# Kernel optimization log

Measured on AMD Instinct MI355X. Metric: run time of the kernel, lower is better.

Reference implementation:

```python
import jax, jax.numpy as jnp
import numpy as np

B, H, W, C, G = 256, 64, 64, 3, 128
MH, INV = 10, 18
AS = MH + INV  # 28
EPS = 1e-5


def _bn(x, g, b):
    # training-mode BatchNorm2d: batch stats over (N,H,W), biased variance
    m = x.mean((0, 2, 3), keepdims=True)
    v = x.var((0, 2, 3), keepdims=True)
    return (x - m) * jax.lax.rsqrt(v + EPS) * g.reshape(1, -1, 1, 1) + b.reshape(1, -1, 1, 1)


def _ln(x, g, b):
    m = x.mean(-1, keepdims=True)
    v = x.var(-1, keepdims=True)
    return (x - m) * jax.lax.rsqrt(v + EPS) * g + b


def _conv(x, w, pad):
    return jax.lax.conv_general_dilated(x, w, (1, 1), [(pad, pad), (pad, pad)],
                                        dimension_numbers=('NCHW', 'OIHW', 'NCHW'))


def setup_inputs() -> dict:
    key = jax.random.key(0)
    ks = jax.random.split(key, 24)
    r = lambda i, shape, s=1.0: jax.random.normal(ks[i], shape, jnp.float32) * s
    return {
        'agent_state': r(0, (B, AS)),
        'world_state': r(1, (B, C, H, W)),
        'action': jax.random.uniform(ks[2], (B, 15), jnp.float32, 0.0, 2.999),
        # cnn params
        'bn1_g': jnp.ones((C,), jnp.float32), 'bn1_b': jnp.zeros((C,), jnp.float32),
        'conv1_w': r(3, (G, C, 1, 1), 0.5),
        'bn2_g': jnp.ones((G,), jnp.float32), 'bn2_b': jnp.zeros((G,), jnp.float32),
        'conv2_w': r(4, (G, G, 3, 3), 0.05),
        'bn3_g': jnp.ones((G,), jnp.float32), 'bn3_b': jnp.zeros((G,), jnp.float32),
        'fc1_w': r(5, (20, G), 0.1), 'fc1_b': r(6, (20,), 0.1),
        # mh_inventory
        'ln_mi_g': jnp.ones((AS,), jnp.float32), 'ln_mi_b': jnp.zeros((AS,), jnp.float32),
        'mi_w1': r(7, (100, AS), 0.2), 'mi_w2': r(8, (20, 100), 0.2),
        # action embeddings
        'emb_craft': r(9, (5, 3)), 'emb_equip': r(10, (8, 3)),
        'emb_ncraft': r(11, (8, 3)), 'emb_nsmelt': r(12, (3, 2)), 'emb_place': r(13, (7, 3)),
        # combined_actions
        'ln_ca_g': jnp.ones((24,), jnp.float32), 'ln_ca_b': jnp.zeros((24,), jnp.float32),
        'ca_w1': r(14, (100, 24), 0.2), 'ca_b1': r(15, (100,), 0.1),
        'ca_w2': r(16, (20, 100), 0.2), 'ca_b2': r(17, (20,), 0.1),
        # combined
        'ln_c_g': jnp.ones((60,), jnp.float32), 'ln_c_b': jnp.zeros((60,), jnp.float32),
        'c_w': r(18, (1, 60), 0.2),
        # dist_net
        'ln_d_g': jnp.ones((2 * AS,), jnp.float32), 'ln_d_b': jnp.zeros((2 * AS,), jnp.float32),
        'd_w1': r(19, (50, 2 * AS), 0.2), 'd_w2': r(20, (1, 50), 0.2),
    }


def reference(agent_state, world_state, action,
              bn1_g, bn1_b, conv1_w, bn2_g, bn2_b, conv2_w, bn3_g, bn3_b,
              fc1_w, fc1_b, ln_mi_g, ln_mi_b, mi_w1, mi_w2,
              emb_craft, emb_equip, emb_ncraft, emb_nsmelt, emb_place,
              ln_ca_g, ln_ca_b, ca_w1, ca_b1, ca_w2, ca_b2,
              ln_c_g, ln_c_b, c_w, ln_d_g, ln_d_b, d_w1, d_w2):
    relu = jax.nn.relu
    # ---- CNN branch ----
    x = relu(_bn(world_state, bn1_g, bn1_b))
    x = _conv(x, conv1_w, 0)                      # [B,G,H,W]
    x = relu(_bn(x, bn2_g, bn2_b))
    x = _conv(x, conv2_w, 1)                      # [B,G,H,W]
    x = x.mean((2, 3), keepdims=True)             # AvgPool2d((H,W)) -> [B,G,1,1]
    x = relu(_bn(x, bn3_g, bn3_b)).reshape(x.shape[0], -1)  # [B,G]
    x = relu(x @ fc1_w.T + fc1_b)                 # [B,20]
    # ---- agent-state MLP ----
    y = relu(relu(_ln(agent_state, ln_mi_g, ln_mi_b) @ mi_w1.T) @ mi_w2.T)  # [B,20]
    # ---- per-action embeddings / identities (ModuleDict order) ----
    ai = jax.lax.stop_gradient(action).astype(jnp.int32)
    parts = [action[:, 0:1], action[:, 1:2], action[:, 2:3], action[:, 3:4],
             emb_craft[ai[:, 4]], emb_equip[ai[:, 5]],
             action[:, 6:7], action[:, 7:8], action[:, 8:9],
             emb_ncraft[ai[:, 9]], emb_nsmelt[ai[:, 10]], emb_place[ai[:, 11]],
             action[:, 12:13], action[:, 13:14], action[:, 14:15]]
    acts = jnp.concatenate(parts, axis=1)         # [B,24]
    z = relu(relu(_ln(acts, ln_ca_g, ln_ca_b) @ ca_w1.T + ca_b1) @ ca_w2.T + ca_b2)  # [B,20]
    # ---- combined head ----
    c = jnp.tanh(_ln(jnp.concatenate([x, y, z], axis=1), ln_c_g, ln_c_b) @ c_w.T)    # [B,1]
    # ---- dist_net (previous_agent_state starts as zeros) ----
    prev = jnp.zeros_like(agent_state)
    sc = jnp.concatenate([prev, agent_state], axis=1)  # [B,2*AS]
    d = jnp.tanh(jnp.tanh(_ln(sc, ln_d_g, ln_d_b) @ d_w1.T) @ d_w2.T)                # [B,1]
    return (c, d)
```

## Files before the change

### kernel.cpp

```cpp
#include <hip/hip_runtime.h>
#include <math.h>

#define EPSF 1e-5f

constexpr int OFF_RED1 = 0;
constexpr int OFF_A1B1 = 384;
constexpr int OFF_RED2 = 512;
constexpr int OFF_W2E  = 4096;
constexpr int OFF_M    = OFF_W2E + 128 * 128 * 9;

__device__ __forceinline__ float wave_sum(float v) {
    #pragma unroll
    for (int off = 32; off > 0; off >>= 1) v += __shfl_down(v, off);
    return v;
}

__global__ __launch_bounds__(256) void kA(const float* __restrict__ x,
                                          const float* __restrict__ w2,
                                          float* __restrict__ red1,
                                          float* __restrict__ w2e) {
    int blk = blockIdx.x, tid = threadIdx.x;
    if (blk < 192) {
        int c = blk % 3, seg = blk / 3;
        float s = 0.f, s2 = 0.f;
        for (int bb = 0; bb < 4; ++bb) {
            int b = seg * 4 + bb;
            const float4* p = (const float4*)(x + (size_t)(b * 3 + c) * 4096);
            for (int i = tid; i < 1024; i += 256) {
                float4 v = p[i];
                s += v.x + v.y + v.z + v.w;
                s2 = fmaf(v.x, v.x, s2); s2 = fmaf(v.y, v.y, s2);
                s2 = fmaf(v.z, v.z, s2); s2 = fmaf(v.w, v.w, s2);
            }
        }
        __shared__ float ls[4], ls2[4];
        float ws_ = wave_sum(s), ws2_ = wave_sum(s2);
        if ((tid & 63) == 0) { ls[tid >> 6] = ws_; ls2[tid >> 6] = ws2_; }
        __syncthreads();
        if (tid == 0) {
            red1[blk * 2 + 0] = ls[0] + ls[1] + ls[2] + ls[3];
            red1[blk * 2 + 1] = ls2[0] + ls2[1] + ls2[2] + ls2[3];
        }
    } else {
        int idx = (blk - 192) * 256 + tid;
        int g = idx >> 7, gp = idx & 127;
        const float* wp = w2 + (size_t)(g * 128 + gp) * 9;
        float v0 = wp[0], v1 = wp[1], v2 = wp[2], v3 = wp[3], v4 = wp[4],
              v5 = wp[5], v6 = wp[6], v7 = wp[7], v8 = wp[8];
        float c[9];
        c[0] = ((v0 + v1) + (v2 + v3)) + ((v4 + v5) + (v6 + v7)) + v8;
        c[1] = -(v6 + v7 + v8);
        c[2] = -(v0 + v1 + v2);
        c[3] = -(v2 + v5 + v8);
        c[4] = -(v0 + v3 + v6);
        c[5] = v8; c[6] = v6; c[7] = v2; c[8] = v0;
        #pragma unroll
        for (int k = 0; k < 9; ++k) {
            int jj = gp * 9 + k;
            w2e[(size_t)(jj >> 2) * 512 + g * 4 + (jj & 3)] = c[k];
        }
    }
}

__global__ __launch_bounds__(256) void kB(const float* __restrict__ x,
                                          const float* __restrict__ red1,
                                          const float* __restrict__ g1,
                                          const float* __restrict__ b1,
                                          float* __restrict__ red2,
                                          float* __restrict__ a1b1) {
    __shared__ float ab[6];
    int b = blockIdx.x, tid = threadIdx.x;
    if (tid < 3) {
        float s = 0.f, s2 = 0.f;
        for (int seg = 0; seg < 64; ++seg) {
            s  += red1[(seg * 3 + tid) * 2 + 0];
            s2 += red1[(seg * 3 + tid) * 2 + 1];
        }
        float n = 256.f * 4096.f;
        float mean = s / n, var = s2 / n - mean * mean;
        float a = g1[tid] * rsqrtf(var + EPSF);
        ab[tid] = a; ab[3 + tid] = b1[tid] - mean * a;
        if (b == 0) { a1b1[tid] = a; a1b1[3 + tid] = ab[3 + tid]; }
    }
    __syncthreads();
    float A0 = ab[0], A1 = ab[1], A2 = ab[2];
    float B0 = ab[3], B1 = ab[4], B2 = ab[5];
    float acc[9] = {0, 0, 0, 0, 0, 0, 0, 0, 0};
    const float4* p0 = (const float4*)(x + (size_t)(b * 3 + 0) * 4096);
    const float4* p1 = (const float4*)(x + (size_t)(b * 3 + 1) * 4096);
    const float4* p2 = (const float4*)(x + (size_t)(b * 3 + 2) * 4096);
    for (int i = tid; i < 1024; i += 256) {
        float4 v0 = p0[i], v1 = p1[i], v2 = p2[i];
        #define MOM(e) { \
            float t0 = fmaxf(0.f, fmaf(A0, v0.e, B0)); \
            float t1 = fmaxf(0.f, fmaf(A1, v1.e, B1)); \
            float t2 = fmaxf(0.f, fmaf(A2, v2.e, B2)); \
            acc[0] += t0; acc[1] += t1; acc[2] += t2; \
            acc[3] = fmaf(t0, t0, acc[3]); acc[4] = fmaf(t0, t1, acc[4]); \
            acc[5] = fmaf(t0, t2, acc[5]); acc[6] = fmaf(t1, t1, acc[6]); \
            acc[7] = fmaf(t1, t2, acc[7]); acc[8] = fmaf(t2, t2, acc[8]); }
        MOM(x) MOM(y) MOM(z) MOM(w)
        #undef MOM
    }
    __shared__ float lw[4][9];
    #pragma unroll
    for (int k = 0; k < 9; ++k) {
        float v = wave_sum(acc[k]);
        if ((tid & 63) == 0) lw[tid >> 6][k] = v;
    }
    __syncthreads();
    if (tid == 0) {
        #pragma unroll
        for (int k = 0; k < 9; ++k)
            red2[b * 9 + k] = lw[0][k] + lw[1][k] + lw[2][k] + lw[3][k];
    }
}

__global__ __launch_bounds__(512) void kC(const float* __restrict__ x,
                                          const float* __restrict__ red2,
                                          const float* __restrict__ w1,
                                          const float* __restrict__ g2,
                                          const float* __restrict__ b2,
                                          const float* __restrict__ a1b1,
                                          const float* __restrict__ w2e,
                                          float* __restrict__ m) {
    __shared__ __align__(16) float lds[12288];
    __shared__ __align__(16) float Fsh[1152];
    __shared__ float wt[384], bt[128], momp[288], mom[9], ab[6];
    int b = blockIdx.x, tid = threadIdx.x;
    if (tid < 6) ab[tid] = a1b1[tid];
    if (tid < 288) {
        int seg = tid / 9, k = tid - seg * 9;
        float s = 0.f;
        #pragma unroll
        for (int r = 0; r < 8; ++r) s += red2[(seg * 8 + r) * 9 + k];
        momp[tid] = s;
    }
    __syncthreads();
    if (tid < 9) {
        float s = 0.f;
        #pragma unroll
        for (int sg = 0; sg < 32; ++sg) s += momp[sg * 9 + tid];
        mom[tid] = s / (256.f * 4096.f);
    }
    {
        float A0 = ab[0], A1 = ab[1], A2 = ab[2];
        float B0 = ab[3], B1 = ab[4], B2 = ab[5];
        const float4* xb = (const float4*)(x + (size_t)b * 3 * 4096);
        for (int i = tid; i < 3072; i += 512) {
            float4 v = xb[i];
            int c = i >> 10;
            float a = (c == 0) ? A0 : ((c == 1) ? A1 : A2);
            float bb = (c == 0) ? B0 : ((c == 1) ? B1 : B2);
            v.x = fmaxf(0.f, fmaf(a, v.x, bb));
            v.y = fmaxf(0.f, fmaf(a, v.y, bb));
            v.z = fmaxf(0.f, fmaf(a, v.z, bb));
            v.w = fmaxf(0.f, fmaf(a, v.w, bb));
            *(float4*)&lds[i << 2] = v;
        }
    }
    __syncthreads();
    if (tid < 128) {
        int g = tid;
        float wa = w1[g * 3 + 0], wb = w1[g * 3 + 1], wc = w1[g * 3 + 2];
        float mean = wa * mom[0] + wb * mom[1] + wc * mom[2];
        float ey2 = wa * wa * mom[3] + wb * wb * mom[6] + wc * wc * mom[8]
                  + 2.f * (wa * wb * mom[4] + wa * wc * mom[5] + wb * wc * mom[7]);
        float var = ey2 - mean * mean;
        float a = g2[g] * rsqrtf(var + EPSF);
        wt[g * 3 + 0] = a * wa; wt[g * 3 + 1] = a * wb; wt[g * 3 + 2] = a * wc;
        bt[g] = b2[g] - mean * a;
    }
    __syncthreads();
    int gl = tid & 31, q = tid >> 5;
    {
        float w0[4], w1v[4], w2v[4], bw[4], S[4] = {0, 0, 0, 0};
        #pragma unroll
        for (int j = 0; j < 4; ++j) {
            int g = gl + 32 * j;
            w0[j] = wt[g * 3 + 0]; w1v[j] = wt[g * 3 + 1];
            w2v[j] = wt[g * 3 + 2]; bw[j] = bt[g];
        }
        int base = q * 256;
        #pragma unroll 4
        for (int i = 0; i < 64; ++i) {
            int pp = base + i * 4;
            float4 t0 = *(const float4*)&lds[pp];
            float4 t1 = *(const float4*)&lds[4096 + pp];
            float4 t2 = *(const float4*)&lds[8192 + pp];
            #pragma unroll
            for (int j = 0; j < 4; ++j) {
                float u0 = fmaxf(0.f, fmaf(w0[j], t0.x, fmaf(w1v[j], t1.x, fmaf(w2v[j], t2.x, bw[j]))));
                float u1 = fmaxf(0.f, fmaf(w0[j], t0.y, fmaf(w1v[j], t1.y, fmaf(w2v[j], t2.y, bw[j]))));
                float u2 = fmaxf(0.f, fmaf(w0[j], t0.z, fmaf(w1v[j], t1.z, fmaf(w2v[j], t2.z, bw[j]))));
                float u3 = fmaxf(0.f, fmaf(w0[j], t0.w, fmaf(w1v[j], t1.w, fmaf(w2v[j], t2.w, bw[j]))));
                S[j] += (u0 + u1) + (u2 + u3);
            }
        }
        {
            int g = tid & 127, task = tid >> 7;
            float vw0 = wt[g * 3 + 0], vw1 = wt[g * 3 + 1], vw2 = wt[g * 3 + 2], vb = bt[g];
            float s = 0.f, first = 0.f, last = 0.f;
            int p0 = (task == 1) ? 63 * 64 : ((task == 3) ? 63 : 0);
            int stp = (task >= 2) ? 64 : 1;
            #pragma unroll 4
            for (int i = 0; i < 64; ++i) {
                int p = p0 + i * stp;
                float u = fmaxf(0.f, fmaf(vw0, lds[p], fmaf(vw1, lds[4096 + p], fmaf(vw2, lds[8192 + p], vb))));
                s += u;
                if (i == 0) first = u;
                if (i == 63) last = u;
            }
            Fsh[g * 9 + 1 + task] = s;
            if (task == 0) { Fsh[g * 9 + 5] = first; Fsh[g * 9 + 6] = last; }
            if (task == 1) { Fsh[g * 9 + 7] = first; Fsh[g * 9 + 8] = last; }
        }
        __syncthreads();
        #pragma unroll
        for (int j = 0; j < 4; ++j) lds[(gl + 32 * j) * 17 + q] = S[j];
    }
    __syncthreads();
    if (tid < 128) {
        float s = 0.f;
        #pragma unroll
        for (int qq = 0; qq < 16; ++qq) s += lds[tid * 17 + qq];
        Fsh[tid * 9 + 0] = s;
    }
    __syncthreads();
    {
        int chunk = tid >> 7, g = tid & 127;
        float acc = 0.f;
        #pragma unroll 4
        for (int t = 0; t < 72; ++t) {
            int jb = chunk * 72 + t;
            float4 wv = *(const float4*)&w2e[(size_t)jb * 512 + g * 4];
            float4 fv = *(const float4*)&Fsh[jb * 4];
            acc = fmaf(wv.x, fv.x, fmaf(wv.y, fv.y, fmaf(wv.z, fv.z, fmaf(wv.w, fv.w, acc))));
        }
        __syncthreads();
        lds[chunk * 128 + g] = acc;
    }
    __syncthreads();
    if (tid < 128)
        m[b * 128 + tid] = (lds[tid] + lds[128 + tid] + lds[256 + tid] + lds[384 + tid]) * (1.f / 4096.f);
}

__global__ __launch_bounds__(256) void kE(
    const float* __restrict__ m, const float* __restrict__ g3, const float* __restrict__ b3,
    const float* __restrict__ agent, const float* __restrict__ action,
    const float* __restrict__ fc1w, const float* __restrict__ fc1b,
    const float* __restrict__ lnmig, const float* __restrict__ lnmib,
    const float* __restrict__ miw1, const float* __restrict__ miw2,
    const float* __restrict__ embc, const float* __restrict__ embe,
    const float* __restrict__ embnc, const float* __restrict__ embns,
    const float* __restrict__ embp,
    const float* __restrict__ lncag, const float* __restrict__ lncab,
    const float* __restrict__ caw1, const float* __restrict__ cab1,
    const float* __restrict__ caw2, const float* __restrict__ cab2,
    const float* __restrict__ lncg, const float* __restrict__ lncb,
    const float* __restrict__ cw,
    const float* __restrict__ lndg, const float* __restrict__ lndb,
    const float* __restrict__ dw1, const float* __restrict__ dw2,
    float* __restrict__ out) {
    __shared__ float red[4][128];
    __shared__ float xsh[128];
    __shared__ float lnv[28], lnca[24], lnsc[56], h1[100], h2[100], h3[50], cat[60];
    int b = blockIdx.x, tid = threadIdx.x;
    {
        int g = tid & 127, half = tid >> 7;
        float s = 0.f, s2 = 0.f;
        for (int i = 0; i < 128; ++i) {
            float v = m[(half * 128 + i) * 128 + g];
            s += v; s2 = fmaf(v, v, s2);
        }
        red[half * 2 + 0][g] = s;
        red[half * 2 + 1][g] = s2;
    }
    __syncthreads();
    if (tid < 128) {
        float s = red[0][tid] + red[2][tid], s2 = red[1][tid] + red[3][tid];
        float mean = s / 256.f, var = s2 / 256.f - mean * mean;
        float a = g3[tid] * rsqrtf(var + EPSF);
        float bb = b3[tid] - mean * a;
        xsh[tid] = fmaxf(0.f, fmaf(a, m[b * 128 + tid], bb));
    }
    int l = tid & 63, w = tid >> 6;
    if (w == 0) {
        float av = (l < 28) ? agent[b * 28 + l] : 0.f;
        float s = wave_sum(av), s2 = wave_sum(av * av);
        s = __shfl(s, 0); s2 = __shfl(s2, 0);
        float mean = s / 28.f, var = s2 / 28.f - mean * mean;
        float rs = rsqrtf(var + EPSF);
        if (l < 28) lnv[l] = (av - mean) * rs * lnmig[l] + lnmib[l];
    } else if (w == 1) {
        const float* ab = action + b * 15;
        float actv = 0.f;
        if (l < 24) {
            if (l < 4)       actv = ab[l];
            else if (l < 7)  { int ix = (int)ab[4];  actv = embc[ix * 3 + (l - 4)]; }
            else if (l < 10) { int ix = (int)ab[5];  actv = embe[ix * 3 + (l - 7)]; }
            else if (l < 13) actv = ab[l - 4];
            else if (l < 16) { int ix = (int)ab[9];  actv = embnc[ix * 3 + (l - 13)]; }
            else if (l < 18) { int ix = (int)ab[10]; actv = embns[ix * 2 + (l - 16)]; }
            else if (l < 21) { int ix = (int)ab[11]; actv = embp[ix * 3 + (l - 18)]; }
            else             actv = ab[l - 9];
        }
        float s = wave_sum(actv), s2 = wave_sum(actv * actv);
        s = __shfl(s, 0); s2 = __shfl(s2, 0);
        float mean = s / 24.f, var = s2 / 24.f - mean * mean;
        float rs = rsqrtf(var + EPSF);
        if (l < 24) lnca[l] = (actv - mean) * rs * lncag[l] + lncab[l];
    } else if (w == 2) {
        float g1v = (l < 56) ? agent[b * 28 + (l < 28 ? l : l - 28)] : 0.f;
        float av = (l < 28) ? g1v : 0.f;
        float s = wave_sum(av), s2 = wave_sum(av * av);
        s = __shfl(s, 0); s2 = __shfl(s2, 0);
        float mean = s / 56.f, var = s2 / 56.f - mean * mean;
        float rs = rsqrtf(var + EPSF);
        if (l < 56) {
            float vv = (l < 28) ? 0.f : g1v;
            lnsc[l] = (vv - mean) * rs * lndg[l] + lndb[l];
        }
    }
    __syncthreads();
    if (tid < 100) {
        float a = 0.f;
        for (int i = 0; i < 28; ++i) a = fmaf(miw1[tid * 28 + i], lnv[i], a);
        h1[tid] = fmaxf(0.f, a);
    } else if (tid < 200) {
        int j = tid - 100;
        float a = cab1[j];
        for (int i = 0; i < 24; ++i) a = fmaf(caw1[j * 24 + i], lnca[i], a);
        h2[j] = fmaxf(0.f, a);
    } else if (tid < 250) {
        int j = tid - 200;
        float a = 0.f;
        for (int i = 0; i < 56; ++i) a = fmaf(dw1[j * 56 + i], lnsc[i], a);
        h3[j] = tanhf(a);
    }
    __syncthreads();
    if (tid < 20) {
        float a = 0.f;
        for (int i = 0; i < 100; ++i) a = fmaf(miw2[tid * 100 + i], h1[i], a);
        cat[20 + tid] = fmaxf(0.f, a);
    } else if (tid >= 64 && tid < 84) {
        int j = tid - 64;
        float a = cab2[j];
        for (int i = 0; i < 100; ++i) a = fmaf(caw2[j * 100 + i], h2[i], a);
        cat[40 + j] = fmaxf(0.f, a);
    } else if (tid >= 128 && tid < 148) {
        int j = tid - 128;
        float a = fc1b[j];
        for (int i = 0; i < 128; ++i) a = fmaf(fc1w[j * 128 + i], xsh[i], a);
        cat[j] = fmaxf(0.f, a);
    } else if (tid >= 192) {
        int l3 = tid - 192;
        float dt = (l3 < 50) ? dw2[l3] * h3[l3] : 0.f;
        dt = wave_sum(dt);
        if (l3 == 0) out[256 + b] = tanhf(dt);
    }
    __syncthreads();
    if (w == 0) {
        float cv = (l < 60) ? cat[l] : 0.f;
        float ss = wave_sum(cv), ss2 = wave_sum(cv * cv);
        ss = __shfl(ss, 0); ss2 = __shfl(ss2, 0);
        float mean60 = ss / 60.f, var60 = ss2 / 60.f - mean60 * mean60;
        float rs60 = rsqrtf(var60 + EPSF);
        float term = (l < 60) ? cw[l] * ((cv - mean60) * rs60 * lncg[l] + lncb[l]) : 0.f;
        term = wave_sum(term);
        if (l == 0) out[b] = tanhf(term);
    }
}

extern "C" void kernel_launch(void* const* d_in, const int* in_sizes, int n_in,
                              void* d_out, int out_size, void* d_ws, size_t ws_size,
                              hipStream_t stream) {
    (void)in_sizes; (void)n_in; (void)out_size; (void)ws_size;
    const float* agent  = (const float*)d_in[0];
    const float* world  = (const float*)d_in[1];
    const float* action = (const float*)d_in[2];
    const float* bn1_g  = (const float*)d_in[3];
    const float* bn1_b  = (const float*)d_in[4];
    const float* conv1w = (const float*)d_in[5];
    const float* bn2_g  = (const float*)d_in[6];
    const float* bn2_b  = (const float*)d_in[7];
    const float* conv2w = (const float*)d_in[8];
    const float* bn3_g  = (const float*)d_in[9];
    const float* bn3_b  = (const float*)d_in[10];
    const float* fc1w   = (const float*)d_in[11];
    const float* fc1b   = (const float*)d_in[12];
    const float* lnmig  = (const float*)d_in[13];
    const float* lnmib  = (const float*)d_in[14];
    const float* miw1   = (const float*)d_in[15];
    const float* miw2   = (const float*)d_in[16];
    const float* embc   = (const float*)d_in[17];
    const float* embe   = (const float*)d_in[18];
    const float* embnc  = (const float*)d_in[19];
    const float* embns  = (const float*)d_in[20];
    const float* embp   = (const float*)d_in[21];
    const float* lncag  = (const float*)d_in[22];
    const float* lncab  = (const float*)d_in[23];
    const float* caw1   = (const float*)d_in[24];
    const float* cab1   = (const float*)d_in[25];
    const float* caw2   = (const float*)d_in[26];
    const float* cab2   = (const float*)d_in[27];
    const float* lncg   = (const float*)d_in[28];
    const float* lncb   = (const float*)d_in[29];
    const float* cw     = (const float*)d_in[30];
    const float* lndg   = (const float*)d_in[31];
    const float* lndb   = (const float*)d_in[32];
    const float* dw1    = (const float*)d_in[33];
    const float* dw2    = (const float*)d_in[34];
    float* out = (float*)d_out;
    float* ws = (float*)d_ws;

    hipLaunchKernelGGL(kA, dim3(256), dim3(256), 0, stream,
                       world, conv2w, ws + OFF_RED1, ws + OFF_W2E);
    hipLaunchKernelGGL(kB, dim3(256), dim3(256), 0, stream,
                       world, ws + OFF_RED1, bn1_g, bn1_b, ws + OFF_RED2, ws + OFF_A1B1);
    hipLaunchKernelGGL(kC, dim3(256), dim3(512), 0, stream,
                       world, ws + OFF_RED2, conv1w, bn2_g, bn2_b, ws + OFF_A1B1,
                       ws + OFF_W2E, ws + OFF_M);
    hipLaunchKernelGGL(kE, dim3(256), dim3(256), 0, stream,
                       ws + OFF_M, bn3_g, bn3_b, agent, action, fc1w, fc1b,
                       lnmig, lnmib, miw1, miw2,
                       embc, embe, embnc, embns, embp,
                       lncag, lncab, caw1, cab1, caw2, cab2,
                       lncg, lncb, cw, lndg, lndb, dw1, dw2, out);
}
```

Before: 186.3 us.

## Fuse four kernels into one cooperative kernel with grid syncs

Replaces the four-kernel pipeline with a single cooperative kernel of 256 blocks by 512 threads that uses grid.sync between the BN-stat, moment, conv and head stages. Each block keeps its batch item's normalized input in shared memory, so the second pass over the world tensor in the conv stage is no longer needed. This removes launch gaps and some global traffic, but needs all 256 blocks co-resident and adds grid-wide barrier cost. If the cooperative launch fails, it falls back to the old kernels.

```diff
diff --git a/kernel.cpp b/kernel.cpp
--- a/kernel.cpp
+++ b/kernel.cpp
@@ -1,5 +1,8 @@
 #include <hip/hip_runtime.h>
+#include <hip/hip_cooperative_groups.h>
 #include <math.h>
+
+namespace cg = cooperative_groups;
 
 #define EPSF 1e-5f
 
@@ -13,6 +16,335 @@
     #pragma unroll
     for (int off = 32; off > 0; off >>= 1) v += __shfl_down(v, off);
     return v;
+}
+
+struct KParams {
+    const float *agent, *world, *action;
+    const float *bn1_g, *bn1_b, *conv1w, *bn2_g, *bn2_b, *conv2w, *bn3_g, *bn3_b;
+    const float *fc1w, *fc1b, *lnmig, *lnmib, *miw1, *miw2;
+    const float *embc, *embe, *embnc, *embns, *embp;
+    const float *lncag, *lncab, *caw1, *cab1, *caw2, *cab2;
+    const float *lncg, *lncb, *cw, *lndg, *lndb, *dw1, *dw2;
+    float *out, *ws;
+};
+
+__global__ __launch_bounds__(512, 2) void fused(KParams p) {
+    cg::grid_group grid = cg::this_grid();
+    const int blk = blockIdx.x, tid = threadIdx.x;
+    float* red1 = p.ws + OFF_RED1;
+    float* red2 = p.ws + OFF_RED2;
+    float* w2e  = p.ws + OFF_W2E;
+    float* m    = p.ws + OFF_M;
+
+    __shared__ __align__(16) float T[12288];
+    __shared__ __align__(16) float Fsh[1152];
+    __shared__ float wt[384], bt[128], momp[288], mom[9], ab[6];
+    __shared__ float wred[8][9], lss[8], lss2[8], mrow[128];
+    __shared__ float xsh[128], lnv[28], lnca[24], lnsc[56], h1[100], h2[100], h3[50], cat[60];
+
+    if (blk < 192) {
+        int c = blk % 3, seg = blk / 3;
+        float s = 0.f, s2 = 0.f;
+        #pragma unroll
+        for (int bb = 0; bb < 4; ++bb) {
+            const float4* q = (const float4*)(p.world + (size_t)((seg * 4 + bb) * 3 + c) * 4096);
+            for (int i = tid; i < 1024; i += 512) {
+                float4 v = q[i];
+                s += (v.x + v.y) + (v.z + v.w);
+                s2 = fmaf(v.x, v.x, s2); s2 = fmaf(v.y, v.y, s2);
+                s2 = fmaf(v.z, v.z, s2); s2 = fmaf(v.w, v.w, s2);
+            }
+        }
+        float a = wave_sum(s), b2_ = wave_sum(s2);
+        if ((tid & 63) == 0) { lss[tid >> 6] = a; lss2[tid >> 6] = b2_; }
+        __syncthreads();
+        if (tid == 0) {
+            float ts = 0.f, ts2 = 0.f;
+            #pragma unroll
+            for (int wv = 0; wv < 8; ++wv) { ts += lss[wv]; ts2 += lss2[wv]; }
+            red1[blk * 2 + 0] = ts; red1[blk * 2 + 1] = ts2;
+        }
+    } else if (tid < 256) {
+        int idx = (blk - 192) * 256 + tid;
+        int g = idx >> 7, gp = idx & 127;
+        const float* wp = p.conv2w + (size_t)(g * 128 + gp) * 9;
+        float v0 = wp[0], v1 = wp[1], v2 = wp[2], v3 = wp[3], v4 = wp[4],
+              v5 = wp[5], v6 = wp[6], v7 = wp[7], v8 = wp[8];
+        float c9[9];
+        c9[0] = ((v0 + v1) + (v2 + v3)) + ((v4 + v5) + (v6 + v7)) + v8;
+        c9[1] = -(v6 + v7 + v8);
+        c9[2] = -(v0 + v1 + v2);
+        c9[3] = -(v2 + v5 + v8);
+        c9[4] = -(v0 + v3 + v6);
+        c9[5] = v8; c9[6] = v6; c9[7] = v2; c9[8] = v0;
+        #pragma unroll
+        for (int k = 0; k < 9; ++k) {
+            int jj = gp * 9 + k;
+            w2e[(size_t)(jj >> 2) * 512 + g * 4 + (jj & 3)] = c9[k];
+        }
+    }
+    grid.sync();
+
+    const int b = blk;
+    if (tid < 3) {
+        float s = 0.f, s2 = 0.f;
+        for (int seg = 0; seg < 64; ++seg) {
+            s  += red1[(seg * 3 + tid) * 2 + 0];
+            s2 += red1[(seg * 3 + tid) * 2 + 1];
+        }
+        float n = 256.f * 4096.f;
+        float mean = s / n, var = s2 / n - mean * mean;
+        float a = p.bn1_g[tid] * rsqrtf(var + EPSF);
+        ab[tid] = a; ab[3 + tid] = p.bn1_b[tid] - mean * a;
+    }
+    __syncthreads();
+    {
+        float A0 = ab[0], A1 = ab[1], A2 = ab[2];
+        float B0 = ab[3], B1 = ab[4], B2 = ab[5];
+        const float4* p0 = (const float4*)(p.world + (size_t)(b * 3 + 0) * 4096);
+        const float4* p1 = (const float4*)(p.world + (size_t)(b * 3 + 1) * 4096);
+        const float4* p2 = (const float4*)(p.world + (size_t)(b * 3 + 2) * 4096);
+        float acc[9] = {0, 0, 0, 0, 0, 0, 0, 0, 0};
+        for (int i = tid; i < 1024; i += 512) {
+            float4 v0 = p0[i], v1 = p1[i], v2 = p2[i];
+            float4 t0, t1, t2;
+            #define MOM(e) { \
+                float u0 = fmaxf(0.f, fmaf(A0, v0.e, B0)); \
+                float u1 = fmaxf(0.f, fmaf(A1, v1.e, B1)); \
+                float u2 = fmaxf(0.f, fmaf(A2, v2.e, B2)); \
+                t0.e = u0; t1.e = u1; t2.e = u2; \
+                acc[0] += u0; acc[1] += u1; acc[2] += u2; \
+                acc[3] = fmaf(u0, u0, acc[3]); acc[4] = fmaf(u0, u1, acc[4]); \
+                acc[5] = fmaf(u0, u2, acc[5]); acc[6] = fmaf(u1, u1, acc[6]); \
+                acc[7] = fmaf(u1, u2, acc[7]); acc[8] = fmaf(u2, u2, acc[8]); }
+            MOM(x) MOM(y) MOM(z) MOM(w)
+            #undef MOM
+            *(float4*)&T[i * 4]        = t0;
+            *(float4*)&T[4096 + i * 4] = t1;
+            *(float4*)&T[8192 + i * 4] = t2;
+        }
+        #pragma unroll
+        for (int k = 0; k < 9; ++k) {
+            float v = wave_sum(acc[k]);
+            if ((tid & 63) == 0) wred[tid >> 6][k] = v;
+        }
+        __syncthreads();
+        if (tid < 9) {
+            float s = 0.f;
+            #pragma unroll
+            for (int wv = 0; wv < 8; ++wv) s += wred[wv][tid];
+            red2[b * 9 + tid] = s;
+        }
+    }
+    grid.sync();
+
+    if (tid < 288) {
+        int seg = tid / 9, k = tid - seg * 9;
+        float s = 0.f;
+        #pragma unroll
+        for (int r = 0; r < 8; ++r) s += red2[(seg * 8 + r) * 9 + k];
+        momp[tid] = s;
+    }
+    __syncthreads();
+    if (tid < 9) {
+        float s = 0.f;
+        #pragma unroll
+        for (int sg = 0; sg < 32; ++sg) s += momp[sg * 9 + tid];
+        mom[tid] = s / (256.f * 4096.f);
+    }
+    __syncthreads();
+    if (tid < 128) {
+        int g = tid;
+        float wa = p.conv1w[g * 3 + 0], wb = p.conv1w[g * 3 + 1], wc = p.conv1w[g * 3 + 2];
+        float mean = wa * mom[0] + wb * mom[1] + wc * mom[2];
+        float ey2 = wa * wa * mom[3] + wb * wb * mom[6] + wc * wc * mom[8]
+                  + 2.f * (wa * wb * mom[4] + wa * wc * mom[5] + wb * wc * mom[7]);
+        float var = ey2 - mean * mean;
+        float a = p.bn2_g[g] * rsqrtf(var + EPSF);
+        wt[g * 3 + 0] = a * wa; wt[g * 3 + 1] = a * wb; wt[g * 3 + 2] = a * wc;
+        bt[g] = p.bn2_b[g] - mean * a;
+    }
+    __syncthreads();
+    int gl = tid & 31, qc = tid >> 5;
+    {
+        float w0[4], w1v[4], w2v[4], bw[4], S[4] = {0, 0, 0, 0};
+        #pragma unroll
+        for (int j = 0; j < 4; ++j) {
+            int g = gl + 32 * j;
+            w0[j] = wt[g * 3 + 0]; w1v[j] = wt[g * 3 + 1];
+            w2v[j] = wt[g * 3 + 2]; bw[j] = bt[g];
+        }
+        int base = qc * 256;
+        #pragma unroll 4
+        for (int i = 0; i < 64; ++i) {
+            int pp = base + i * 4;
+            float4 t0 = *(const float4*)&T[pp];
+            float4 t1 = *(const float4*)&T[4096 + pp];
+            float4 t2 = *(const float4*)&T[8192 + pp];
+            #pragma unroll
+            for (int j = 0; j < 4; ++j) {
+                float u0 = fmaxf(0.f, fmaf(w0[j], t0.x, fmaf(w1v[j], t1.x, fmaf(w2v[j], t2.x, bw[j]))));
+                float u1 = fmaxf(0.f, fmaf(w0[j], t0.y, fmaf(w1v[j], t1.y, fmaf(w2v[j], t2.y, bw[j]))));
+                float u2 = fmaxf(0.f, fmaf(w0[j], t0.z, fmaf(w1v[j], t1.z, fmaf(w2v[j], t2.z, bw[j]))));
+                float u3 = fmaxf(0.f, fmaf(w0[j], t0.w, fmaf(w1v[j], t1.w, fmaf(w2v[j], t2.w, bw[j]))));
+                S[j] += (u0 + u1) + (u2 + u3);
+            }
+        }
+        {
+            int g = tid & 127, task = tid >> 7;
+            float vw0 = wt[g * 3 + 0], vw1 = wt[g * 3 + 1], vw2 = wt[g * 3 + 2], vb = bt[g];
+            float s = 0.f, first = 0.f, last = 0.f;
+            int p0 = (task == 1) ? 63 * 64 : ((task == 3) ? 63 : 0);
+            int stp = (task >= 2) ? 64 : 1;
+            #pragma unroll 4
+            for (int i = 0; i < 64; ++i) {
+                int pp = p0 + i * stp;
+                float u = fmaxf(0.f, fmaf(vw0, T[pp], fmaf(vw1, T[4096 + pp], fmaf(vw2, T[8192 + pp], vb))));
+                s += u;
+                if (i == 0) first = u;
+                if (i == 63) last = u;
+            }
+            Fsh[g * 9 + 1 + task] = s;
+            if (task == 0) { Fsh[g * 9 + 5] = first; Fsh[g * 9 + 6] = last; }
+            if (task == 1) { Fsh[g * 9 + 7] = first; Fsh[g * 9 + 8] = last; }
+        }
+        __syncthreads();
+        #pragma unroll
+        for (int j = 0; j < 4; ++j) T[(gl + 32 * j) * 17 + qc] = S[j];
+    }
+    __syncthreads();
+    if (tid < 128) {
+        float s = 0.f;
+        #pragma unroll
+        for (int qq = 0; qq < 16; ++qq) s += T[tid * 17 + qq];
+        Fsh[tid * 9 + 0] = s;
+    }
+    __syncthreads();
+    {
+        int chunk = tid >> 7, g = tid & 127;
+        float acc = 0.f;
+        #pragma unroll 4
+        for (int t = 0; t < 72; ++t) {
+            int jb = chunk * 72 + t;
+            float4 wv = *(const float4*)&w2e[(size_t)jb * 512 + g * 4];
+            float4 fv = *(const float4*)&Fsh[jb * 4];
+            acc = fmaf(wv.x, fv.x, fmaf(wv.y, fv.y, fmaf(wv.z, fv.z, fmaf(wv.w, fv.w, acc))));
+        }
+        __syncthreads();
+        T[chunk * 128 + g] = acc;
+    }
+    __syncthreads();
+    if (tid < 128) {
+        float v = (T[tid] + T[128 + tid] + T[256 + tid] + T[384 + tid]) * (1.f / 4096.f);
+        m[b * 128 + tid] = v;
+        mrow[tid] = v;
+    }
+    grid.sync();
+
+    {
+        int g = tid & 127, qtr = tid >> 7;
+        float s = 0.f, s2 = 0.f;
+        for (int i = 0; i < 64; ++i) {
+            float v = m[(qtr * 64 + i) * 128 + g];
+            s += v; s2 = fmaf(v, v, s2);
+        }
+        T[tid] = s; T[512 + tid] = s2;
+    }
+    __syncthreads();
+    if (tid < 128) {
+        float s  = T[tid] + T[128 + tid] + T[256 + tid] + T[384 + tid];
+        float s2 = T[512 + tid] + T[640 + tid] + T[768 + tid] + T[896 + tid];
+        float mean = s / 256.f, var = s2 / 256.f - mean * mean;
+        float a = p.bn3_g[tid] * rsqrtf(var + EPSF);
+        float bb = p.bn3_b[tid] - mean * a;
+        xsh[tid] = fmaxf(0.f, fmaf(a, mrow[tid], bb));
+    }
+    int l = tid & 63, w = tid >> 6;
+    if (w == 0) {
+        float av = (l < 28) ? p.agent[b * 28 + l] : 0.f;
+        float s = wave_sum(av), s2 = wave_sum(av * av);
+        s = __shfl(s, 0); s2 = __shfl(s2, 0);
+        float mean = s / 28.f, var = s2 / 28.f - mean * mean;
+        float rs = rsqrtf(var + EPSF);
+        if (l < 28) lnv[l] = (av - mean) * rs * p.lnmig[l] + p.lnmib[l];
+    } else if (w == 1) {
+        const float* ap = p.action + b * 15;
+        float actv = 0.f;
+        if (l < 24) {
+            if (l < 4)       actv = ap[l];
+            else if (l < 7)  { int ix = (int)ap[4];  actv = p.embc[ix * 3 + (l - 4)]; }
+            else if (l < 10) { int ix = (int)ap[5];  actv = p.embe[ix * 3 + (l - 7)]; }
+            else if (l < 13) actv = ap[l - 4];
+            else if (l < 16) { int ix = (int)ap[9];  actv = p.embnc[ix * 3 + (l - 13)]; }
+            else if (l < 18) { int ix = (int)ap[10]; actv = p.embns[ix * 2 + (l - 16)]; }
+            else if (l < 21) { int ix = (int)ap[11]; actv = p.embp[ix * 3 + (l - 18)]; }
+            else             actv = ap[l - 9];
+        }
+        float s = wave_sum(actv), s2 = wave_sum(actv * actv);
+        s = __shfl(s, 0); s2 = __shfl(s2, 0);
+        float mean = s / 24.f, var = s2 / 24.f - mean * mean;
+        float rs = rsqrtf(var + EPSF);
+        if (l < 24) lnca[l] = (actv - mean) * rs * p.lncag[l] + p.lncab[l];
+    } else if (w == 2) {
+        float g1v = (l < 56) ? p.agent[b * 28 + (l < 28 ? l : l - 28)] : 0.f;
+        float av = (l < 28) ? g1v : 0.f;
+        float s = wave_sum(av), s2 = wave_sum(av * av);
+        s = __shfl(s, 0); s2 = __shfl(s2, 0);
+        float mean = s / 56.f, var = s2 / 56.f - mean * mean;
+        float rs = rsqrtf(var + EPSF);
+        if (l < 56) {
+            float vv = (l < 28) ? 0.f : g1v;
+            lnsc[l] = (vv - mean) * rs * p.lndg[l] + p.lndb[l];
+        }
+    }
+    __syncthreads();
+    if (tid < 100) {
+        float a = 0.f;
+        for (int i = 0; i < 28; ++i) a = fmaf(p.miw1[tid * 28 + i], lnv[i], a);
+        h1[tid] = fmaxf(0.f, a);
+    } else if (tid < 200) {
+        int j = tid - 100;
+        float a = p.cab1[j];
+        for (int i = 0; i < 24; ++i) a = fmaf(p.caw1[j * 24 + i], lnca[i], a);
+        h2[j] = fmaxf(0.f, a);
+    } else if (tid < 250) {
+        int j = tid - 200;
+        float a = 0.f;
+        for (int i = 0; i < 56; ++i) a = fmaf(p.dw1[j * 56 + i], lnsc[i], a);
+        h3[j] = tanhf(a);
+    }
+    __syncthreads();
+    if (tid < 20) {
+        float a = 0.f;
+        for (int i = 0; i < 100; ++i) a = fmaf(p.miw2[tid * 100 + i], h1[i], a);
+        cat[20 + tid] = fmaxf(0.f, a);
+    } else if (tid >= 64 && tid < 84) {
+        int j = tid - 64;
+        float a = p.cab2[j];
+        for (int i = 0; i < 100; ++i) a = fmaf(p.caw2[j * 100 + i], h2[i], a);
+        cat[40 + j] = fmaxf(0.f, a);
+    } else if (tid >= 128 && tid < 148) {
+        int j = tid - 128;
+        float a = p.fc1b[j];
+        for (int i = 0; i < 128; ++i) a = fmaf(p.fc1w[j * 128 + i], xsh[i], a);
+        cat[j] = fmaxf(0.f, a);
+    } else if (tid >= 192 && tid < 256) {
+        int l3 = tid - 192;
+        float dt = (l3 < 50) ? p.dw2[l3] * h3[l3] : 0.f;
+        dt = wave_sum(dt);
+        if (l3 == 0) p.out[256 + b] = tanhf(dt);
+    }
+    __syncthreads();
+    if (w == 0) {
+        float cv = (l < 60) ? cat[l] : 0.f;
+        float ss = wave_sum(cv), ss2 = wave_sum(cv * cv);
+        ss = __shfl(ss, 0); ss2 = __shfl(ss2, 0);
+        float mean60 = ss / 60.f, var60 = ss2 / 60.f - mean60 * mean60;
+        float rs60 = rsqrtf(var60 + EPSF);
+        float term = (l < 60) ? p.cw[l] * ((cv - mean60) * rs60 * p.lncg[l] + p.lncb[l]) : 0.f;
+        term = wave_sum(term);
+        if (l == 0) p.out[b] = tanhf(term);
+    }
 }
 
 __global__ __launch_bounds__(256) void kA(const float* __restrict__ x,
@@ -376,55 +708,62 @@
                               void* d_out, int out_size, void* d_ws, size_t ws_size,
                               hipStream_t stream) {
     (void)in_sizes; (void)n_in; (void)out_size; (void)ws_size;
-    const float* agent  = (const float*)d_in[0];
-    const float* world  = (const float*)d_in[1];
-    const float* action = (const float*)d_in[2];
-    const float* bn1_g  = (const float*)d_in[3];
-    const float* bn1_b  = (const float*)d_in[4];
-    const float* conv1w = (const float*)d_in[5];
-    const float* bn2_g  = (const float*)d_in[6];
-    const float* bn2_b  = (const float*)d_in[7];
-    const float* conv2w = (const float*)d_in[8];
-    const float* bn3_g  = (const float*)d_in[9];
-    const float* bn3_b  = (const float*)d_in[10];
-    const float* fc1w   = (const float*)d_in[11];
-    const float* fc1b   = (const float*)d_in[12];
-    const float* lnmig  = (const float*)d_in[13];
-    const float* lnmib  = (const float*)d_in[14];
-    const float* miw1   = (const float*)d_in[15];
-    const float* miw2   = (const float*)d_in[16];
-    const float* embc   = (const float*)d_in[17];
-    const float* embe   = (const float*)d_in[18];
-    const float* embnc  = (const float*)d_in[19];
-    const float* embns  = (const float*)d_in[20];
-    const float* embp   = (const float*)d_in[21];
-    const float* lncag  = (const float*)d_in[22];
-    const float* lncab  = (const float*)d_in[23];
-    const float* caw1   = (const float*)d_in[24];
-    const float* cab1   = (const float*)d_in[25];
-    const float* caw2   = (const float*)d_in[26];
-    const float* cab2   = (const float*)d_in[27];
-    const float* lncg   = (const float*)d_in[28];
-    const float* lncb   = (const float*)d_in[29];
-    const float* cw     = (const float*)d_in[30];
-    const float* lndg   = (const float*)d_in[31];
-    const float* lndb   = (const float*)d_in[32];
-    const float* dw1    = (const float*)d_in[33];
-    const float* dw2    = (const float*)d_in[34];
-    float* out = (float*)d_out;
-    float* ws = (float*)d_ws;
-
-    hipLaunchKernelGGL(kA, dim3(256), dim3(256), 0, stream,
-                       world, conv2w, ws + OFF_RED1, ws + OFF_W2E);
-    hipLaunchKernelGGL(kB, dim3(256), dim3(256), 0, stream,
-                       world, ws + OFF_RED1, bn1_g, bn1_b, ws + OFF_RED2, ws + OFF_A1B1);
-    hipLaunchKernelGGL(kC, dim3(256), dim3(512), 0, stream,
-                       world, ws + OFF_RED2, conv1w, bn2_g, bn2_b, ws + OFF_A1B1,
-                       ws + OFF_W2E, ws + OFF_M);
-    hipLaunchKernelGGL(kE, dim3(256), dim3(256), 0, stream,
-                       ws + OFF_M, bn3_g, bn3_b, agent, action, fc1w, fc1b,
-                       lnmig, lnmib, miw1, miw2,
-                       embc, embe, embnc, embns, embp,
-                       lncag, lncab, caw1, cab1, caw2, cab2,
-                       lncg, lncb, cw, lndg, lndb, dw1, dw2, out);
+    KParams hp;
+    hp.agent  = (const float*)d_in[0];
+    hp.world  = (const float*)d_in[1];
+    hp.action = (const float*)d_in[2];
+    hp.bn1_g  = (const float*)d_in[3];
+    hp.bn1_b  = (const float*)d_in[4];
+    hp.conv1w = (const float*)d_in[5];
+    hp.bn2_g  = (const float*)d_in[6];
+    hp.bn2_b  = (const float*)d_in[7];
+    hp.conv2w = (const float*)d_in[8];
+    hp.bn3_g  = (const float*)d_in[9];
+    hp.bn3_b  = (const float*)d_in[10];
+    hp.fc1w   = (const float*)d_in[11];
+    hp.fc1b   = (const float*)d_in[12];
+    hp.lnmig  = (const float*)d_in[13];
+    hp.lnmib  = (const float*)d_in[14];
+    hp.miw1   = (const float*)d_in[15];
+    hp.miw2   = (const float*)d_in[16];
+    hp.embc   = (const float*)d_in[17];
+    hp.embe   = (const float*)d_in[18];
+    hp.embnc  = (const float*)d_in[19];
+    hp.embns  = (const float*)d_in[20];
+    hp.embp   = (const float*)d_in[21];
+    hp.lncag  = (const float*)d_in[22];
+    hp.lncab  = (const float*)d_in[23];
+    hp.caw1   = (const float*)d_in[24];
+    hp.cab1   = (const float*)d_in[25];
+    hp.caw2   = (const float*)d_in[26];
+    hp.cab2   = (const float*)d_in[27];
+    hp.lncg   = (const float*)d_in[28];
+    hp.lncb   = (const float*)d_in[29];
+    hp.cw     = (const float*)d_in[30];
+    hp.lndg   = (const float*)d_in[31];
+    hp.lndb   = (const float*)d_in[32];
+    hp.dw1    = (const float*)d_in[33];
+    hp.dw2    = (const float*)d_in[34];
+    hp.out = (float*)d_out;
+    hp.ws  = (float*)d_ws;
+
+    void* args[] = {&hp};
+    hipError_t err = hipLaunchCooperativeKernel((const void*)fused, dim3(256), dim3(512),
+                                                args, 0, stream);
+    if (err != hipSuccess) {
+        float* ws = hp.ws;
+        hipLaunchKernelGGL(kA, dim3(256), dim3(256), 0, stream,
+                           hp.world, hp.conv2w, ws + OFF_RED1, ws + OFF_W2E);
+        hipLaunchKernelGGL(kB, dim3(256), dim3(256), 0, stream,
+                           hp.world, ws + OFF_RED1, hp.bn1_g, hp.bn1_b, ws + OFF_RED2, ws + OFF_A1B1);
+        hipLaunchKernelGGL(kC, dim3(256), dim3(512), 0, stream,
+                           hp.world, ws + OFF_RED2, hp.conv1w, hp.bn2_g, hp.bn2_b, ws + OFF_A1B1,
+                           ws + OFF_W2E, ws + OFF_M);
+        hipLaunchKernelGGL(kE, dim3(256), dim3(256), 0, stream,
+                           ws + OFF_M, hp.bn3_g, hp.bn3_b, hp.agent, hp.action, hp.fc1w, hp.fc1b,
+                           hp.lnmig, hp.lnmib, hp.miw1, hp.miw2,
+                           hp.embc, hp.embe, hp.embnc, hp.embns, hp.embp,
+                           hp.lncag, hp.lncab, hp.caw1, hp.cab1, hp.caw2, hp.cab2,
+                           hp.lncg, hp.lncb, hp.cw, hp.lndg, hp.lndb, hp.dw1, hp.dw2, hp.out);
+    }
 }
```

Measured after the change: 308.3 us. +65.5%, slower.
